# Performance work log

Measured on AMD Instinct MI355X. Metric: run time of the kernel, lower is better.

The kernel has to match this reference:

```python
import jax, jax.numpy as jnp
import numpy as np

EPS = 1e-8

def setup_inputs() -> dict:
    key = jax.random.key(0)
    k1, k2, k3 = jax.random.split(key, 3)
    b, c, h, w = 64, 20, 128, 128
    x = jax.random.normal(k1, (b, c, h, w), dtype=jnp.float32)
    y = jax.random.randint(k2, (b, c), 0, 2).astype(jnp.int32)
    threshold_p = jnp.zeros((b, c, h * w), dtype=jnp.float32)
    fg = jax.random.uniform(k3, (b, c), dtype=jnp.float32)
    return {"x": x, "y": y, "threshold_p": threshold_p, "fg": fg, "iter": 0}

def reference(x, y, threshold_p, fg, iter):
    b, c, h, w = x.shape
    hw = h * w
    xs = jax.nn.sigmoid(x.reshape(b, c, hw))  # [b,c,hw]
    yf = y.astype(xs.dtype)
    if iter % 100 < 80:
        # per-row descending sort, pick the fg*(h*w)-th value as threshold
        srt = -jnp.sort(-xs.reshape(b * c, hw), axis=1)  # descending
        idx = (fg.reshape(-1) * hw).astype(jnp.int32)  # [b*c]
        thr = jnp.take_along_axis(srt, idx[:, None], axis=1).reshape(b, c, 1)
        thr = jax.lax.stop_gradient(thr)
    else:
        thr = jax.nn.sigmoid(jnp.mean(threshold_p.reshape(b, c, hw), axis=2))[:, :, None]
        xs = jax.lax.stop_gradient(xs)
    thr = jnp.clip(thr, 0.0001)  # [b,c,1], broadcasts over hw
    y_ = yf[:, :, None]  # [b,c,1] broadcast equivalent of stacking hw copies
    mask_low = jax.lax.stop_gradient((xs <= thr).astype(xs.dtype) * y_)
    mask_high = jax.lax.stop_gradient((xs > thr).astype(xs.dtype) * y_)
    h_low = (-(xs * xs) / (thr * thr) + 2.0 * xs / thr) * mask_low
    alpha = 1.0 / jnp.clip((1.0 - thr) ** 2, EPS)
    h_high = alpha * (1.0 - xs) * (1.0 - 2.0 * thr + xs) * mask_high
    if iter % 100 < 80:
        neg_loss = -(1.0 - y_) * jnp.log(jnp.clip(1.0 - xs, EPS))
        loss = jnp.mean(h_high + h_low + neg_loss)
    else:
        loss = jnp.sum(h_low) / jnp.sum(mask_low) + jnp.sum(h_high) / jnp.sum(mask_high)
    return loss
```

## Files before the change

kernel.cpp:

```cpp
#include <hip/hip_runtime.h>

#define HW     16384
#define NROWS  1280
#define NT     512
#define NWAVES (NT / 64)
#define CAP    1536
#define MAXB   128

__device__ __forceinline__ unsigned f2u(float f) {
    unsigned u = __float_as_uint(f);
    unsigned m = (unsigned)((int)u >> 31);
    return u ^ (m | 0x80000000u);
}
__device__ __forceinline__ float u2f(unsigned u) {
    u = (u & 0x80000000u) ? (u & 0x7fffffffu) : ~u;
    return __uint_as_float(u);
}

__device__ __forceinline__ float norminv(float p) {
    const float a1=-3.969683028665376e+01f,a2=2.209460984245205e+02f,
                a3=-2.759285104469687e+02f,a4=1.383577518672690e+02f,
                a5=-3.066479806614716e+01f,a6=2.506628277459239e+00f;
    const float b1=-5.447609879822406e+01f,b2=1.615858368580409e+02f,
                b3=-1.556989798598866e+02f,b4=6.680131188771972e+01f,
                b5=-1.328068155288572e+01f;
    const float c1=-7.784894002430293e-03f,c2=-3.223964580411365e-01f,
                c3=-2.400758277161838e+00f,c4=-2.549732539343734e+00f,
                c5=4.374664141464968e+00f,c6=2.938163982698783e+00f;
    const float d1=7.784695709041462e-03f,d2=3.224671290700398e-01f,
                d3=2.445134137142996e+00f,d4=3.754408661907416e+00f;
    const float plow = 0.02425f;
    float q, r;
    if (p < plow) {
        q = sqrtf(-2.f * logf(p));
        return (((((c1*q+c2)*q+c3)*q+c4)*q+c5)*q+c6) /
               ((((d1*q+d2)*q+d3)*q+d4)*q+1.f);
    } else if (p <= 1.f - plow) {
        q = p - 0.5f; r = q * q;
        return (((((a1*r+a2)*r+a3)*r+a4)*r+a5)*r+a6)*q /
               (((((b1*r+b2)*r+b3)*r+b4)*r+b5)*r+1.f);
    } else {
        q = sqrtf(-2.f * logf(1.f - p));
        return -(((((c1*q+c2)*q+c3)*q+c4)*q+c5)*q+c6) /
                ((((d1*q+d2)*q+d3)*q+d4)*q+1.f);
    }
}

__device__ __forceinline__ void block_scan_pick(
    const unsigned* h, int bpl, unsigned kk,
    volatile unsigned* s_bin, volatile unsigned* s_k, unsigned* wtot)
{
    const int tid  = threadIdx.x;
    const int lane = tid & 63;
    const int wid  = tid >> 6;
    const int base = tid * bpl;
    unsigned local = 0;
    for (int j = 0; j < bpl; ++j) local += h[base + j];
    unsigned s = local;
    #pragma unroll
    for (int off = 1; off < 64; off <<= 1) {
        unsigned t = __shfl_down(s, off, 64);
        if (lane + off < 64) s += t;
    }
    if (lane == 0) wtot[wid] = s;
    __syncthreads();
    unsigned aw = 0;
    #pragma unroll
    for (int w = 0; w < NWAVES; ++w) if (w > wid) aw += wtot[w];
    const unsigned above = aw + (s - local);
    if (above <= kk && above + local > kk) {
        unsigned run = above;
        for (int j = bpl - 1; j >= 0; --j) {
            unsigned c = h[base + j];
            if (run + c > kk) { *s_bin = (unsigned)(base + j); *s_k = kk - run; break; }
            run += c;
        }
    }
    __syncthreads();
}

__global__ __launch_bounds__(NT) void spatial_bce_row(
    const float* __restrict__ x, const int* __restrict__ y,
    const float* __restrict__ fg, double* __restrict__ partial)
{
    __shared__ unsigned hist[4096];
    __shared__ unsigned buf[CAP];
    __shared__ unsigned buf2[MAXB];
    __shared__ unsigned wtot[NWAVES];
    __shared__ unsigned s_cnt, s_cnt2, s_bin, s_k, s_val;
    __shared__ float    swf[NWAVES][6];
    __shared__ double   swd[NWAVES];

    const int row  = blockIdx.x;
    const int tid  = threadIdx.x;
    const int lane = tid & 63;
    const int wid  = tid >> 6;
    const float4* x4 = (const float4*)(x + (size_t)row * HW);
    const float L2E   = 1.44269504f;
    const float LN2   = 0.69314718f;
    const float NLCAP = 18.420680744f;

    const int yrow = y[row];

    if (yrow == 0) {
        float a0 = 0.f, a1 = 0.f, a2 = 0.f, a3 = 0.f;
        for (int i = tid; i < HW / 4; i += NT) {
            float4 v = x4[i];
            a0 += fminf(fmaxf(v.x, 0.f) + LN2 * log2f(1.f + exp2f(-L2E * fabsf(v.x))), NLCAP);
            a1 += fminf(fmaxf(v.y, 0.f) + LN2 * log2f(1.f + exp2f(-L2E * fabsf(v.y))), NLCAP);
            a2 += fminf(fmaxf(v.z, 0.f) + LN2 * log2f(1.f + exp2f(-L2E * fabsf(v.z))), NLCAP);
            a3 += fminf(fmaxf(v.w, 0.f) + LN2 * log2f(1.f + exp2f(-L2E * fabsf(v.w))), NLCAP);
        }
        double acc = (double)((a0 + a1) + (a2 + a3));
        #pragma unroll
        for (int off = 32; off > 0; off >>= 1) acc += __shfl_down(acc, off, 64);
        if (lane == 0) swd[wid] = acc;
        __syncthreads();
        if (tid == 0) {
            double t = 0.0;
            for (int w = 0; w < NWAVES; ++w) t += swd[w];
            partial[row] = t;
        }
        return;
    }

    int k = (int)(fg[row] * (float)HW);
    k = max(0, min(HW - 1, k));
    const unsigned ku = (unsigned)k;
    const float pq  = 1.f - ((float)k + 0.5f) * (1.f / (float)HW);
    const float z   = norminv(pq);
    const float phi = 0.39894228f * exp2f(-0.72134752f * z * z);
    const float sig = sqrtf(pq * (1.f - pq) * (1.f / (float)HW)) / phi;
    const float dl  = 6.f * sig + 0.02f;
    const float fa  = z + dl, fb = z - dl;
    const unsigned ua = f2u(fa), ub = f2u(fb);

    {
        uint4 zz = {0u, 0u, 0u, 0u};
        for (int i = tid; i < 1024 / 4; i += NT) ((uint4*)hist)[i] = zz;
    }
    if (tid == 0) { s_cnt = 0u; s_cnt2 = 0u; }
    __syncthreads();

    float t1a = 0.f, t2a = 0.f, gaa = 0.f, g2aa = 0.f, cafa = 0.f, cbfa = 0.f;
    float t1b = 0.f, t2b = 0.f, gab = 0.f, g2ab = 0.f, cafb = 0.f, cbfb = 0.f;
    for (int i = tid; i < HW / 4; i += 2 * NT) {
        float4 v0 = x4[i];
        float4 v1 = x4[i + NT];
        float e0[4] = {v0.x, v0.y, v0.z, v0.w};
        float e1[4] = {v1.x, v1.y, v1.z, v1.w};
        #pragma unroll
        for (int j = 0; j < 4; ++j) {
            float xv = e0[j];
            unsigned u = f2u(xv);
            float s = __builtin_amdgcn_rcpf(1.f + exp2f(-L2E * xv));
            float s2 = s * s;
            t1a += s; t2a += s2;
            if (u > ua) { gaa += s; g2aa += s2; cafa += 1.f; }
            if (u > ub) {
                cbfa += 1.f;
                if (u <= ua) { unsigned p = atomicAdd(&s_cnt, 1u); if (p < CAP) buf[p] = u; }
            }
        }
        #pragma unroll
        for (int j = 0; j < 4; ++j) {
            float xv = e1[j];
            unsigned u = f2u(xv);
            float s = __builtin_amdgcn_rcpf(1.f + exp2f(-L2E * xv));
            float s2 = s * s;
            t1b += s; t2b += s2;
            if (u > ua) { gab += s; g2ab += s2; cafb += 1.f; }
            if (u > ub) {
                cbfb += 1.f;
                if (u <= ua) { unsigned p = atomicAdd(&s_cnt, 1u); if (p < CAP) buf[p] = u; }
            }
        }
    }
    float t1 = t1a + t1b, t2 = t2a + t2b;
    float ga = gaa + gab, g2a = g2aa + g2ab;
    float caf = cafa + cafb, cbf = cbfa + cbfb;
    #pragma unroll
    for (int off = 32; off > 0; off >>= 1) {
        t1  += __shfl_down(t1,  off, 64);
        t2  += __shfl_down(t2,  off, 64);
        ga  += __shfl_down(ga,  off, 64);
        g2a += __shfl_down(g2a, off, 64);
        caf += __shfl_down(caf, off, 64);
        cbf += __shfl_down(cbf, off, 64);
    }
    if (lane == 0) {
        swf[wid][0] = t1;  swf[wid][1] = t2;  swf[wid][2] = ga;
        swf[wid][3] = g2a; swf[wid][4] = caf; swf[wid][5] = cbf;
    }
    __syncthreads();
    double dS1 = 0, dS2 = 0, dGa = 0, dG2a = 0, dCa = 0, dCb = 0;
    #pragma unroll
    for (int w = 0; w < NWAVES; ++w) {
        dS1 += swf[w][0]; dS2 += swf[w][1]; dGa  += swf[w][2];
        dG2a += swf[w][3]; dCa += swf[w][4]; dCb += swf[w][5];
    }
    const unsigned ca  = (unsigned)(dCa + 0.5);
    const unsigned cb  = (unsigned)(dCb + 0.5);
    const unsigned cnt = s_cnt;
    const unsigned UCLIP = f2u(-9.2102404f);
    const bool valid = (ca <= ku) && (ku < cb) && (cnt <= CAP);

    unsigned ustar;
    bool addSide;
    float hs = 0.f, hs2 = 0.f, hn = 0.f;

    if (valid) {
        const float scale = 1024.f / (fa - fb);
        for (int c = tid; c < (int)cnt; c += NT) {
            float xv = u2f(buf[c]);
            int bn = (int)((xv - fb) * scale);
            bn = max(0, min(1023, bn));
            atomicAdd(&hist[bn], 1u);
        }
        __syncthreads();
        const unsigned kp = ku - ca;
        block_scan_pick(hist, 1024 / NT, kp, &s_bin, &s_k, wtot);
        const unsigned binv = s_bin;
        const unsigned kin  = s_k;
        for (int c = tid; c < (int)cnt; c += NT) {
            unsigned u = buf[c];
            float xv = u2f(u);
            int bn = (int)((xv - fb) * scale);
            bn = max(0, min(1023, bn));
            if (bn == (int)binv) { unsigned p = atomicAdd(&s_cnt2, 1u); if (p < MAXB) buf2[p] = u; }
        }
        __syncthreads();
        const unsigned m = s_cnt2;
        if (m <= MAXB) {
            for (int i = tid; i < (int)m; i += NT) {
                unsigned v = buf2[i];
                unsigned gt = 0, eq = 0;
                for (int j = 0; j < (int)m; ++j) {
                    unsigned w = buf2[j];
                    gt += (w > v); eq += (w == v);
                }
                if (gt <= kin && kin < gt + eq) s_val = v;
            }
        } else {
            for (int c = tid; c < (int)cnt; c += NT) {
                unsigned v = buf[c];
                unsigned gt = 0, eq = 0;
                for (int j = 0; j < (int)cnt; ++j) {
                    unsigned w = buf[j];
                    gt += (w > v); eq += (w == v);
                }
                if (gt <= kp && kp < gt + eq) s_val = v;
            }
        }
        __syncthreads();
        ustar = s_val;

        if (ustar >= UCLIP) {
            addSide = true;
            for (int c = tid; c < (int)cnt; c += NT) {
                unsigned u = buf[c];
                if (u > ustar) {
                    float xv = u2f(u);
                    float s = __builtin_amdgcn_rcpf(1.f + exp2f(-L2E * xv));
                    hs += s; hs2 += s * s; hn += 1.f;
                }
            }
        } else {
            addSide = false;
            for (int i = tid; i < HW / 4; i += NT) {
                float4 v = x4[i];
                float e[4] = {v.x, v.y, v.z, v.w};
                #pragma unroll
                for (int j = 0; j < 4; ++j) {
                    if (f2u(e[j]) > UCLIP) {
                        float s = __builtin_amdgcn_rcpf(1.f + exp2f(-L2E * e[j]));
                        hs += s; hs2 += s * s; hn += 1.f;
                    }
                }
            }
        }
    } else {
        {
            uint4 zz = {0u, 0u, 0u, 0u};
            for (int i = tid; i < 4096 / 4; i += NT) ((uint4*)hist)[i] = zz;
        }
        __syncthreads();
        for (int i = tid; i < HW / 4; i += NT) {
            float4 v = x4[i];
            atomicAdd(&hist[f2u(v.x) >> 20], 1u);
            atomicAdd(&hist[f2u(v.y) >> 20], 1u);
            atomicAdd(&hist[f2u(v.z) >> 20], 1u);
            atomicAdd(&hist[f2u(v.w) >> 20], 1u);
        }
        __syncthreads();
        block_scan_pick(hist, 4096 / NT, ku, &s_bin, &s_k, wtot);
        const unsigned bin1 = s_bin;
        const unsigned k1   = s_k;
        for (int i = tid; i < 2048; i += NT) hist[i] = 0u;
        __syncthreads();
        for (int i = tid; i < HW / 4; i += NT) {
            float4 v = x4[i];
            unsigned u[4] = {f2u(v.x), f2u(v.y), f2u(v.z), f2u(v.w)};
            #pragma unroll
            for (int j = 0; j < 4; ++j)
                if ((u[j] >> 20) == bin1) atomicAdd(&hist[(u[j] >> 10) & 1023u], 1u);
        }
        __syncthreads();
        block_scan_pick(hist, 1024 / NT, k1, &s_bin, &s_k, wtot);
        const unsigned pfx22 = (bin1 << 10) | s_bin;
        const unsigned k2    = s_k;
        for (int i = tid; i < HW / 4; i += NT) {
            float4 v = x4[i];
            unsigned u[4] = {f2u(v.x), f2u(v.y), f2u(v.z), f2u(v.w)};
            #pragma unroll
            for (int j = 0; j < 4; ++j)
                if ((u[j] >> 10) == pfx22) atomicAdd(&hist[1024 + (u[j] & 1023u)], 1u);
        }
        __syncthreads();
        block_scan_pick(hist + 1024, 1024 / NT, k2, &s_bin, &s_k, wtot);
        ustar = (pfx22 << 10) | s_bin;

        addSide = false;
        const unsigned uthr = max(ustar, UCLIP);
        for (int i = tid; i < HW / 4; i += NT) {
            float4 v = x4[i];
            float e[4] = {v.x, v.y, v.z, v.w};
            #pragma unroll
            for (int j = 0; j < 4; ++j) {
                if (f2u(e[j]) > uthr) {
                    float s = __builtin_amdgcn_rcpf(1.f + exp2f(-L2E * e[j]));
                    hs += s; hs2 += s * s; hn += 1.f;
                }
            }
        }
    }

    #pragma unroll
    for (int off = 32; off > 0; off >>= 1) {
        hs  += __shfl_down(hs,  off, 64);
        hs2 += __shfl_down(hs2, off, 64);
        hn  += __shfl_down(hn,  off, 64);
    }
    if (lane == 0) { swf[wid][0] = hs; swf[wid][1] = hs2; swf[wid][2] = hn; }
    __syncthreads();
    if (tid == 0) {
        double HS = 0, HS2 = 0, HN = 0;
        for (int w = 0; w < NWAVES; ++w) {
            HS += swf[w][0]; HS2 += swf[w][1]; HN += swf[w][2];
        }
        double SH, S2H, NH;
        if (addSide) { SH = dGa + HS; S2H = dG2a + HS2; NH = dCa + HN; }
        else         { SH = HS;       S2H = HS2;        NH = HN; }
        const double SL = dS1 - SH, S2L = dS2 - S2H;

        const float xk = u2f(ustar);
        float thrf = 1.0f / (1.0f + expf(-xk));
        thrf = fmaxf(thrf, 1e-4f);
        const double t   = (double)thrf;
        const double omt = 1.0 - t;
        const double al  = 1.0 / fmax(omt * omt, 1e-8);
        partial[row] = 2.0 * SL / t - S2L / (t * t)
                     + al * (NH * (1.0 - 2.0 * t) + 2.0 * t * SH - S2H);
    }
}

__global__ __launch_bounds__(256) void spatial_bce_final(
    const double* __restrict__ partial, float* __restrict__ out)
{
    __shared__ double sred[256];
    double acc = 0.0;
    for (int i = threadIdx.x; i < NROWS; i += 256) acc += partial[i];
    sred[threadIdx.x] = acc;
    __syncthreads();
    for (int off = 128; off > 0; off >>= 1) {
        if (threadIdx.x < off) sred[threadIdx.x] += sred[threadIdx.x + off];
        __syncthreads();
    }
    if (threadIdx.x == 0)
        out[0] = (float)(sred[0] / ((double)NROWS * (double)HW));
}

extern "C" void kernel_launch(void* const* d_in, const int* in_sizes, int n_in,
                              void* d_out, int out_size, void* d_ws, size_t ws_size,
                              hipStream_t stream) {
    const float* x  = (const float*)d_in[0];
    const int*   y  = (const int*)d_in[1];
    const float* fg = (const float*)d_in[3];

    double* partial = (double*)d_ws;

    spatial_bce_row<<<NROWS, NT, 0, stream>>>(x, y, fg, partial);
    spatial_bce_final<<<1, 256, 0, stream>>>(partial, (float*)d_out);
}
```

Baseline: 38.38 us.

## Split each row across two blocks with a candidate-buffer finalize kernel

Replaces the single per-row kernel with a two-stage scheme. A streaming pass runs two 256-thread blocks per row, each computing partial sigmoid moments and collecting bracket candidates into global memory. A finalize kernel then selects the k-th value from the merged candidates. A monolithic fallback kernel with a replicated radix histogram is kept for when the workspace is too small. The goal is more blocks in flight for better occupancy and bandwidth, at the cost of an extra kernel launch and global round-trips for moments and candidates.

```diff
diff --git a/kernel.cpp b/kernel.cpp
--- a/kernel.cpp
+++ b/kernel.cpp
@@ -2,10 +2,8 @@
 
 #define HW     16384
 #define NROWS  1280
-#define NT     512
-#define NWAVES (NT / 64)
-#define CAP    1536
-#define MAXB   128
+#define CAPH   1024
+#define MB     256
 
 __device__ __forceinline__ unsigned f2u(float f) {
     unsigned u = __float_as_uint(f);
@@ -46,16 +44,30 @@
     }
 }
 
+__device__ __forceinline__ void bracket_ab(int k, float* fa, float* fb) {
+    const float pq  = 1.f - ((float)k + 0.5f) * (1.f / (float)HW);
+    const float z   = norminv(pq);
+    const float phi = 0.39894228f * exp2f(-0.72134752f * z * z);
+    const float sig = sqrtf(pq * (1.f - pq) * (1.f / (float)HW)) / phi;
+    const float dl  = 6.f * sig + 0.02f;
+    *fa = z + dl; *fb = z - dl;
+}
+
+template<int NTH>
 __device__ __forceinline__ void block_scan_pick(
-    const unsigned* h, int bpl, unsigned kk,
+    const unsigned* h, int bpl, int stride, unsigned kk,
     volatile unsigned* s_bin, volatile unsigned* s_k, unsigned* wtot)
 {
+    constexpr int NW = NTH / 64;
     const int tid  = threadIdx.x;
     const int lane = tid & 63;
     const int wid  = tid >> 6;
     const int base = tid * bpl;
     unsigned local = 0;
-    for (int j = 0; j < bpl; ++j) local += h[base + j];
+    for (int j = 0; j < bpl; ++j) {
+        int b = base + j;
+        local += h[stride * b] + (stride == 2 ? h[stride * b + 1] : 0u);
+    }
     unsigned s = local;
     #pragma unroll
     for (int off = 1; off < 64; off <<= 1) {
@@ -66,45 +78,44 @@
     __syncthreads();
     unsigned aw = 0;
     #pragma unroll
-    for (int w = 0; w < NWAVES; ++w) if (w > wid) aw += wtot[w];
+    for (int w = 0; w < NW; ++w) if (w > wid) aw += wtot[w];
     const unsigned above = aw + (s - local);
     if (above <= kk && above + local > kk) {
         unsigned run = above;
         for (int j = bpl - 1; j >= 0; --j) {
-            unsigned c = h[base + j];
-            if (run + c > kk) { *s_bin = (unsigned)(base + j); *s_k = kk - run; break; }
+            int b = base + j;
+            unsigned c = h[stride * b] + (stride == 2 ? h[stride * b + 1] : 0u);
+            if (run + c > kk) { *s_bin = (unsigned)b; *s_k = kk - run; break; }
             run += c;
         }
     }
     __syncthreads();
 }
 
-__global__ __launch_bounds__(NT) void spatial_bce_row(
+__global__ __launch_bounds__(256) void stream_pass(
     const float* __restrict__ x, const int* __restrict__ y,
-    const float* __restrict__ fg, double* __restrict__ partial)
+    const float* __restrict__ fg, double* __restrict__ mom,
+    unsigned* __restrict__ cnts, unsigned* __restrict__ cand)
 {
-    __shared__ unsigned hist[4096];
-    __shared__ unsigned buf[CAP];
-    __shared__ unsigned buf2[MAXB];
-    __shared__ unsigned wtot[NWAVES];
-    __shared__ unsigned s_cnt, s_cnt2, s_bin, s_k, s_val;
-    __shared__ float    swf[NWAVES][6];
-    __shared__ double   swd[NWAVES];
-
-    const int row  = blockIdx.x;
+    __shared__ unsigned sbuf[CAPH];
+    __shared__ unsigned s_cnt;
+    __shared__ float    swf[4][6];
+    __shared__ double   swd[4];
+
+    const int bid  = blockIdx.x;
+    const int row  = bid >> 1;
+    const int half = bid & 1;
     const int tid  = threadIdx.x;
     const int lane = tid & 63;
     const int wid  = tid >> 6;
-    const float4* x4 = (const float4*)(x + (size_t)row * HW);
+    const float4* x4 = (const float4*)(x + (size_t)row * HW + half * (HW / 2));
     const float L2E   = 1.44269504f;
     const float LN2   = 0.69314718f;
     const float NLCAP = 18.420680744f;
 
-    const int yrow = y[row];
-
-    if (yrow == 0) {
+    if (y[row] == 0) {
         float a0 = 0.f, a1 = 0.f, a2 = 0.f, a3 = 0.f;
-        for (int i = tid; i < HW / 4; i += NT) {
+        for (int i = tid; i < HW / 8; i += 256) {
             float4 v = x4[i];
             a0 += fminf(fmaxf(v.x, 0.f) + LN2 * log2f(1.f + exp2f(-L2E * fabsf(v.x))), NLCAP);
             a1 += fminf(fmaxf(v.y, 0.f) + LN2 * log2f(1.f + exp2f(-L2E * fabsf(v.y))), NLCAP);
@@ -117,65 +128,53 @@
         if (lane == 0) swd[wid] = acc;
         __syncthreads();
         if (tid == 0) {
-            double t = 0.0;
-            for (int w = 0; w < NWAVES; ++w) t += swd[w];
-            partial[row] = t;
+            double t = swd[0] + swd[1] + swd[2] + swd[3];
+            mom[(size_t)bid * 6] = t;
         }
         return;
     }
 
     int k = (int)(fg[row] * (float)HW);
     k = max(0, min(HW - 1, k));
-    const unsigned ku = (unsigned)k;
-    const float pq  = 1.f - ((float)k + 0.5f) * (1.f / (float)HW);
-    const float z   = norminv(pq);
-    const float phi = 0.39894228f * exp2f(-0.72134752f * z * z);
-    const float sig = sqrtf(pq * (1.f - pq) * (1.f / (float)HW)) / phi;
-    const float dl  = 6.f * sig + 0.02f;
-    const float fa  = z + dl, fb = z - dl;
+    float fa, fb; bracket_ab(k, &fa, &fb);
     const unsigned ua = f2u(fa), ub = f2u(fb);
-
-    {
-        uint4 zz = {0u, 0u, 0u, 0u};
-        for (int i = tid; i < 1024 / 4; i += NT) ((uint4*)hist)[i] = zz;
-    }
-    if (tid == 0) { s_cnt = 0u; s_cnt2 = 0u; }
+    if (tid == 0) s_cnt = 0u;
     __syncthreads();
 
     float t1a = 0.f, t2a = 0.f, gaa = 0.f, g2aa = 0.f, cafa = 0.f, cbfa = 0.f;
     float t1b = 0.f, t2b = 0.f, gab = 0.f, g2ab = 0.f, cafb = 0.f, cbfb = 0.f;
-    for (int i = tid; i < HW / 4; i += 2 * NT) {
+
+#define PROC(xv, T1, T2, GA, G2A, CAF, CBF)                                   \
+    {                                                                         \
+        float _xv = (xv);                                                     \
+        unsigned _u = f2u(_xv);                                               \
+        float _s = __builtin_amdgcn_rcpf(1.f + exp2f(-L2E * _xv));            \
+        float _s2 = _s * _s;                                                  \
+        T1 += _s; T2 += _s2;                                                  \
+        if (_u > ua) { GA += _s; G2A += _s2; CAF += 1.f; }                    \
+        if (_u > ub) {                                                        \
+            CBF += 1.f;                                                       \
+            if (_u <= ua) {                                                   \
+                unsigned _p = atomicAdd(&s_cnt, 1u);                          \
+                if (_p < CAPH) sbuf[_p] = _u;                                 \
+            }                                                                 \
+        }                                                                     \
+    }
+
+    for (int i = tid; i < HW / 8; i += 512) {
         float4 v0 = x4[i];
-        float4 v1 = x4[i + NT];
-        float e0[4] = {v0.x, v0.y, v0.z, v0.w};
-        float e1[4] = {v1.x, v1.y, v1.z, v1.w};
-        #pragma unroll
-        for (int j = 0; j < 4; ++j) {
-            float xv = e0[j];
-            unsigned u = f2u(xv);
-            float s = __builtin_amdgcn_rcpf(1.f + exp2f(-L2E * xv));
-            float s2 = s * s;
-            t1a += s; t2a += s2;
-            if (u > ua) { gaa += s; g2aa += s2; cafa += 1.f; }
-            if (u > ub) {
-                cbfa += 1.f;
-                if (u <= ua) { unsigned p = atomicAdd(&s_cnt, 1u); if (p < CAP) buf[p] = u; }
-            }
-        }
-        #pragma unroll
-        for (int j = 0; j < 4; ++j) {
-            float xv = e1[j];
-            unsigned u = f2u(xv);
-            float s = __builtin_amdgcn_rcpf(1.f + exp2f(-L2E * xv));
-            float s2 = s * s;
-            t1b += s; t2b += s2;
-            if (u > ua) { gab += s; g2ab += s2; cafb += 1.f; }
-            if (u > ub) {
-                cbfb += 1.f;
-                if (u <= ua) { unsigned p = atomicAdd(&s_cnt, 1u); if (p < CAP) buf[p] = u; }
-            }
-        }
-    }
+        float4 v1 = x4[i + 256];
+        PROC(v0.x, t1a, t2a, gaa, g2aa, cafa, cbfa);
+        PROC(v0.y, t1a, t2a, gaa, g2aa, cafa, cbfa);
+        PROC(v0.z, t1a, t2a, gaa, g2aa, cafa, cbfa);
+        PROC(v0.w, t1a, t2a, gaa, g2aa, cafa, cbfa);
+        PROC(v1.x, t1b, t2b, gab, g2ab, cafb, cbfb);
+        PROC(v1.y, t1b, t2b, gab, g2ab, cafb, cbfb);
+        PROC(v1.z, t1b, t2b, gab, g2ab, cafb, cbfb);
+        PROC(v1.w, t1b, t2b, gab, g2ab, cafb, cbfb);
+    }
+#undef PROC
+
     float t1 = t1a + t1b, t2 = t2a + t2b;
     float ga = gaa + gab, g2a = g2aa + g2ab;
     float caf = cafa + cafb, cbf = cbfa + cbfb;
@@ -193,60 +192,110 @@
         swf[wid][3] = g2a; swf[wid][4] = caf; swf[wid][5] = cbf;
     }
     __syncthreads();
-    double dS1 = 0, dS2 = 0, dGa = 0, dG2a = 0, dCa = 0, dCb = 0;
-    #pragma unroll
-    for (int w = 0; w < NWAVES; ++w) {
-        dS1 += swf[w][0]; dS2 += swf[w][1]; dGa  += swf[w][2];
-        dG2a += swf[w][3]; dCa += swf[w][4]; dCb += swf[w][5];
-    }
+    const unsigned cfin = s_cnt;
+    if (tid == 0) {
+        double m0 = 0, m1 = 0, m2 = 0, m3 = 0, m4 = 0, m5 = 0;
+        #pragma unroll
+        for (int w = 0; w < 4; ++w) {
+            m0 += swf[w][0]; m1 += swf[w][1]; m2 += swf[w][2];
+            m3 += swf[w][3]; m4 += swf[w][4]; m5 += swf[w][5];
+        }
+        double* o = mom + (size_t)bid * 6;
+        o[0] = m0; o[1] = m1; o[2] = m2; o[3] = m3; o[4] = m4; o[5] = m5;
+        cnts[bid] = cfin;
+    }
+    const unsigned c = cfin < CAPH ? cfin : CAPH;
+    unsigned* dst = cand + (size_t)bid * CAPH;
+    for (unsigned j = tid; j < c; j += 256) dst[j] = sbuf[j];
+}
+
+__global__ __launch_bounds__(256) void finalize_row(
+    const float* __restrict__ x, const int* __restrict__ y,
+    const float* __restrict__ fg, const double* __restrict__ mom,
+    const unsigned* __restrict__ cnts, const unsigned* __restrict__ cand,
+    double* __restrict__ partial)
+{
+    __shared__ unsigned hist[4096];
+    __shared__ unsigned buf2[MB];
+    __shared__ unsigned wtot[4];
+    __shared__ unsigned s_cnt2, s_bin, s_k, s_val;
+    __shared__ float    swf[4][3];
+
+    const int r    = blockIdx.x;
+    const int tid  = threadIdx.x;
+    const int lane = tid & 63;
+    const int wid  = tid >> 6;
+
+    if (y[r] == 0) {
+        if (tid == 0)
+            partial[r] = mom[(size_t)(2 * r) * 6] + mom[(size_t)(2 * r + 1) * 6];
+        return;
+    }
+
+    const double* mA = mom + (size_t)(2 * r) * 6;
+    const double* mB = mA + 6;
+    const double dS1 = mA[0] + mB[0], dS2 = mA[1] + mB[1];
+    const double dGa = mA[2] + mB[2], dG2a = mA[3] + mB[3];
+    const double dCa = mA[4] + mB[4], dCb = mA[5] + mB[5];
     const unsigned ca  = (unsigned)(dCa + 0.5);
-    const unsigned cb  = (unsigned)(dCb + 0.5);
-    const unsigned cnt = s_cnt;
+    const unsigned cbn = (unsigned)(dCb + 0.5);
+    int k = (int)(fg[r] * (float)HW);
+    k = max(0, min(HW - 1, k));
+    const unsigned ku = (unsigned)k;
+    const unsigned c0 = cnts[2 * r], c1 = cnts[2 * r + 1];
     const unsigned UCLIP = f2u(-9.2102404f);
-    const bool valid = (ca <= ku) && (ku < cb) && (cnt <= CAP);
-
-    unsigned ustar;
-    bool addSide;
-    float hs = 0.f, hs2 = 0.f, hn = 0.f;
+    const bool valid = (ca <= ku) && (ku < cbn) && (c0 <= CAPH) && (c1 <= CAPH);
+    const unsigned* seg0 = cand + (size_t)(2 * r) * CAPH;
+    const unsigned* seg1 = cand + (size_t)(2 * r + 1) * CAPH;
+    const unsigned total = c0 + c1;
+    const float L2E = 1.44269504f;
+
+    unsigned ustar = 0;
+    bool haveU = false;
 
     if (valid) {
+        float fa, fb; bracket_ab(k, &fa, &fb);
         const float scale = 1024.f / (fa - fb);
-        for (int c = tid; c < (int)cnt; c += NT) {
-            float xv = u2f(buf[c]);
-            int bn = (int)((xv - fb) * scale);
+        for (int i = tid; i < 1024; i += 256) hist[i] = 0u;
+        if (tid == 0) s_cnt2 = 0u;
+        __syncthreads();
+        for (unsigned t = tid; t < total; t += 256) {
+            unsigned u = (t < c0) ? seg0[t] : seg1[t - c0];
+            int bn = (int)((u2f(u) - fb) * scale);
             bn = max(0, min(1023, bn));
             atomicAdd(&hist[bn], 1u);
         }
         __syncthreads();
-        const unsigned kp = ku - ca;
-        block_scan_pick(hist, 1024 / NT, kp, &s_bin, &s_k, wtot);
-        const unsigned binv = s_bin;
-        const unsigned kin  = s_k;
-        for (int c = tid; c < (int)cnt; c += NT) {
-            unsigned u = buf[c];
-            float xv = u2f(u);
-            int bn = (int)((xv - fb) * scale);
+        block_scan_pick<256>(hist, 4, 1, ku - ca, &s_bin, &s_k, wtot);
+        const unsigned binv = s_bin, kin = s_k;
+        for (unsigned t = tid; t < total; t += 256) {
+            unsigned u = (t < c0) ? seg0[t] : seg1[t - c0];
+            int bn = (int)((u2f(u) - fb) * scale);
             bn = max(0, min(1023, bn));
-            if (bn == (int)binv) { unsigned p = atomicAdd(&s_cnt2, 1u); if (p < MAXB) buf2[p] = u; }
+            if (bn == (int)binv) {
+                unsigned p = atomicAdd(&s_cnt2, 1u);
+                if (p < MB) buf2[p] = u;
+            }
         }
         __syncthreads();
         const unsigned m = s_cnt2;
-        if (m <= MAXB) {
-            for (int i = tid; i < (int)m; i += NT) {
+        if (m <= MB) {
+            for (unsigned i = tid; i < m; i += 256) {
                 unsigned v = buf2[i];
                 unsigned gt = 0, eq = 0;
-                for (int j = 0; j < (int)m; ++j) {
+                for (unsigned j = 0; j < m; ++j) {
                     unsigned w = buf2[j];
                     gt += (w > v); eq += (w == v);
                 }
                 if (gt <= kin && kin < gt + eq) s_val = v;
             }
         } else {
-            for (int c = tid; c < (int)cnt; c += NT) {
-                unsigned v = buf[c];
+            const unsigned kp = ku - ca;
+            for (unsigned t = tid; t < total; t += 256) {
+                unsigned v = (t < c0) ? seg0[t] : seg1[t - c0];
                 unsigned gt = 0, eq = 0;
-                for (int j = 0; j < (int)cnt; ++j) {
-                    unsigned w = buf[j];
+                for (unsigned j = 0; j < total; ++j) {
+                    unsigned w = (j < c0) ? seg0[j] : seg1[j - c0];
                     gt += (w > v); eq += (w == v);
                 }
                 if (gt <= kp && kp < gt + eq) s_val = v;
@@ -254,75 +303,62 @@
         }
         __syncthreads();
         ustar = s_val;
-
-        if (ustar >= UCLIP) {
-            addSide = true;
-            for (int c = tid; c < (int)cnt; c += NT) {
-                unsigned u = buf[c];
-                if (u > ustar) {
-                    float xv = u2f(u);
-                    float s = __builtin_amdgcn_rcpf(1.f + exp2f(-L2E * xv));
-                    hs += s; hs2 += s * s; hn += 1.f;
-                }
-            }
-        } else {
-            addSide = false;
-            for (int i = tid; i < HW / 4; i += NT) {
+        haveU = true;
+    }
+
+    float hs = 0.f, hs2 = 0.f, hn = 0.f;
+    bool addSide = false;
+    if (haveU && ustar >= UCLIP) {
+        addSide = true;
+        for (unsigned t = tid; t < total; t += 256) {
+            unsigned u = (t < c0) ? seg0[t] : seg1[t - c0];
+            if (u > ustar) {
+                float xv = u2f(u);
+                float s = __builtin_amdgcn_rcpf(1.f + exp2f(-L2E * xv));
+                hs += s; hs2 += s * s; hn += 1.f;
+            }
+        }
+    } else {
+        const float4* x4 = (const float4*)(x + (size_t)r * HW);
+        if (!haveU) {
+            for (int i = tid; i < 4096; i += 256) hist[i] = 0u;
+            __syncthreads();
+            for (int i = tid; i < HW / 4; i += 256) {
                 float4 v = x4[i];
-                float e[4] = {v.x, v.y, v.z, v.w};
+                atomicAdd(&hist[f2u(v.x) >> 20], 1u);
+                atomicAdd(&hist[f2u(v.y) >> 20], 1u);
+                atomicAdd(&hist[f2u(v.z) >> 20], 1u);
+                atomicAdd(&hist[f2u(v.w) >> 20], 1u);
+            }
+            __syncthreads();
+            block_scan_pick<256>(hist, 16, 1, ku, &s_bin, &s_k, wtot);
+            const unsigned bin1 = s_bin, k1 = s_k;
+            for (int i = tid; i < 2048; i += 256) hist[i] = 0u;
+            __syncthreads();
+            for (int i = tid; i < HW / 4; i += 256) {
+                float4 v = x4[i];
+                unsigned uu[4] = {f2u(v.x), f2u(v.y), f2u(v.z), f2u(v.w)};
                 #pragma unroll
-                for (int j = 0; j < 4; ++j) {
-                    if (f2u(e[j]) > UCLIP) {
-                        float s = __builtin_amdgcn_rcpf(1.f + exp2f(-L2E * e[j]));
-                        hs += s; hs2 += s * s; hn += 1.f;
-                    }
-                }
-            }
-        }
-    } else {
-        {
-            uint4 zz = {0u, 0u, 0u, 0u};
-            for (int i = tid; i < 4096 / 4; i += NT) ((uint4*)hist)[i] = zz;
-        }
-        __syncthreads();
-        for (int i = tid; i < HW / 4; i += NT) {
-            float4 v = x4[i];
-            atomicAdd(&hist[f2u(v.x) >> 20], 1u);
-            atomicAdd(&hist[f2u(v.y) >> 20], 1u);
-            atomicAdd(&hist[f2u(v.z) >> 20], 1u);
-            atomicAdd(&hist[f2u(v.w) >> 20], 1u);
-        }
-        __syncthreads();
-        block_scan_pick(hist, 4096 / NT, ku, &s_bin, &s_k, wtot);
-        const unsigned bin1 = s_bin;
-        const unsigned k1   = s_k;
-        for (int i = tid; i < 2048; i += NT) hist[i] = 0u;
-        __syncthreads();
-        for (int i = tid; i < HW / 4; i += NT) {
-            float4 v = x4[i];
-            unsigned u[4] = {f2u(v.x), f2u(v.y), f2u(v.z), f2u(v.w)};
-            #pragma unroll
-            for (int j = 0; j < 4; ++j)
-                if ((u[j] >> 20) == bin1) atomicAdd(&hist[(u[j] >> 10) & 1023u], 1u);
-        }
-        __syncthreads();
-        block_scan_pick(hist, 1024 / NT, k1, &s_bin, &s_k, wtot);
-        const unsigned pfx22 = (bin1 << 10) | s_bin;
-        const unsigned k2    = s_k;
-        for (int i = tid; i < HW / 4; i += NT) {
-            float4 v = x4[i];
-            unsigned u[4] = {f2u(v.x), f2u(v.y), f2u(v.z), f2u(v.w)};
-            #pragma unroll
-            for (int j = 0; j < 4; ++j)
-                if ((u[j] >> 10) == pfx22) atomicAdd(&hist[1024 + (u[j] & 1023u)], 1u);
-        }
-        __syncthreads();
-        block_scan_pick(hist + 1024, 1024 / NT, k2, &s_bin, &s_k, wtot);
-        ustar = (pfx22 << 10) | s_bin;
-
-        addSide = false;
-        const unsigned uthr = max(ustar, UCLIP);
-        for (int i = tid; i < HW / 4; i += NT) {
+                for (int j = 0; j < 4; ++j)
+                    if ((uu[j] >> 20) == bin1) atomicAdd(&hist[(uu[j] >> 10) & 1023u], 1u);
+            }
+            __syncthreads();
+            block_scan_pick<256>(hist, 4, 1, k1, &s_bin, &s_k, wtot);
+            const unsigned pfx22 = (bin1 << 10) | s_bin;
+            const unsigned k2 = s_k;
+            for (int i = tid; i < HW / 4; i += 256) {
+                float4 v = x4[i];
+                unsigned uu[4] = {f2u(v.x), f2u(v.y), f2u(v.z), f2u(v.w)};
+                #pragma unroll
+                for (int j = 0; j < 4; ++j)
+                    if ((uu[j] >> 10) == pfx22) atomicAdd(&hist[1024 + (uu[j] & 1023u)], 1u);
+            }
+            __syncthreads();
+            block_scan_pick<256>(hist + 1024, 4, 1, k2, &s_bin, &s_k, wtot);
+            ustar = (pfx22 << 10) | s_bin;
+        }
+        const unsigned uthr = ustar > UCLIP ? ustar : UCLIP;
+        for (int i = tid; i < HW / 4; i += 256) {
             float4 v = x4[i];
             float e[4] = {v.x, v.y, v.z, v.w};
             #pragma unroll
@@ -345,26 +381,26 @@
     __syncthreads();
     if (tid == 0) {
         double HS = 0, HS2 = 0, HN = 0;
-        for (int w = 0; w < NWAVES; ++w) {
+        #pragma unroll
+        for (int w = 0; w < 4; ++w) {
             HS += swf[w][0]; HS2 += swf[w][1]; HN += swf[w][2];
         }
         double SH, S2H, NH;
         if (addSide) { SH = dGa + HS; S2H = dG2a + HS2; NH = dCa + HN; }
         else         { SH = HS;       S2H = HS2;        NH = HN; }
         const double SL = dS1 - SH, S2L = dS2 - S2H;
-
         const float xk = u2f(ustar);
         float thrf = 1.0f / (1.0f + expf(-xk));
         thrf = fmaxf(thrf, 1e-4f);
         const double t   = (double)thrf;
         const double omt = 1.0 - t;
         const double al  = 1.0 / fmax(omt * omt, 1e-8);
-        partial[row] = 2.0 * SL / t - S2L / (t * t)
-                     + al * (NH * (1.0 - 2.0 * t) + 2.0 * t * SH - S2H);
-    }
-}
-
-__global__ __launch_bounds__(256) void spatial_bce_final(
+        partial[r] = 2.0 * SL / t - S2L / (t * t)
+                   + al * (NH * (1.0 - 2.0 * t) + 2.0 * t * SH - S2H);
+    }
+}
+
+__global__ __launch_bounds__(256) void final_reduce(
     const double* __restrict__ partial, float* __restrict__ out)
 {
     __shared__ double sred[256];
@@ -380,6 +416,199 @@
         out[0] = (float)(sred[0] / ((double)NROWS * (double)HW));
 }
 
+__global__ __launch_bounds__(512) void mono_row(
+    const float* __restrict__ x, const int* __restrict__ y,
+    const float* __restrict__ fg, double* __restrict__ partial)
+{
+    __shared__ unsigned hist[4096 * 2];
+    __shared__ unsigned buf[1024];
+    __shared__ unsigned wtot[8];
+    __shared__ unsigned s_cnt, s_bin, s_k;
+    __shared__ float    swf[8][5];
+    __shared__ double   swd[8];
+
+    const int row  = blockIdx.x;
+    const int tid  = threadIdx.x;
+    const int lane = tid & 63;
+    const int wid  = tid >> 6;
+    const float4* x4 = (const float4*)(x + (size_t)row * HW);
+    const float L2E   = 1.44269504f;
+    const float LN2   = 0.69314718f;
+    const float NLCAP = 18.420680744f;
+
+    const int yrow = y[row];
+
+    if (yrow == 0) {
+        float a0 = 0.f, a1 = 0.f, a2 = 0.f, a3 = 0.f;
+        for (int i = tid; i < HW / 4; i += 512) {
+            float4 v = x4[i];
+            a0 += fminf(fmaxf(v.x, 0.f) + LN2 * log2f(1.f + exp2f(-L2E * fabsf(v.x))), NLCAP);
+            a1 += fminf(fmaxf(v.y, 0.f) + LN2 * log2f(1.f + exp2f(-L2E * fabsf(v.y))), NLCAP);
+            a2 += fminf(fmaxf(v.z, 0.f) + LN2 * log2f(1.f + exp2f(-L2E * fabsf(v.z))), NLCAP);
+            a3 += fminf(fmaxf(v.w, 0.f) + LN2 * log2f(1.f + exp2f(-L2E * fabsf(v.w))), NLCAP);
+        }
+        double acc = (double)((a0 + a1) + (a2 + a3));
+        #pragma unroll
+        for (int off = 32; off > 0; off >>= 1) acc += __shfl_down(acc, off, 64);
+        if (lane == 0) swd[wid] = acc;
+        __syncthreads();
+        if (tid == 0) {
+            double t = 0.0;
+            for (int w = 0; w < 8; ++w) t += swd[w];
+            partial[row] = t;
+        }
+        return;
+    }
+
+    {
+        uint4 z = {0u, 0u, 0u, 0u};
+        for (int i = tid; i < 4096 * 2 / 4; i += 512) ((uint4*)hist)[i] = z;
+    }
+    if (tid == 0) {
+        int k = (int)(fg[row] * (float)HW);
+        k = max(0, min(HW - 1, k));
+        s_k = (unsigned)k; s_cnt = 0u;
+    }
+    __syncthreads();
+    const unsigned k0 = s_k;
+
+    const int rep = tid & 1;
+    for (int i = tid; i < HW / 4; i += 1024) {
+        float4 v0 = x4[i];
+        float4 v1 = x4[i + 512];
+        atomicAdd(&hist[2 * (f2u(v0.x) >> 20) + rep], 1u);
+        atomicAdd(&hist[2 * (f2u(v0.y) >> 20) + rep], 1u);
+        atomicAdd(&hist[2 * (f2u(v0.z) >> 20) + rep], 1u);
+        atomicAdd(&hist[2 * (f2u(v0.w) >> 20) + rep], 1u);
+        atomicAdd(&hist[2 * (f2u(v1.x) >> 20) + rep], 1u);
+        atomicAdd(&hist[2 * (f2u(v1.y) >> 20) + rep], 1u);
+        atomicAdd(&hist[2 * (f2u(v1.z) >> 20) + rep], 1u);
+        atomicAdd(&hist[2 * (f2u(v1.w) >> 20) + rep], 1u);
+    }
+    __syncthreads();
+    block_scan_pick<512>(hist, 4096 / 512, 2, k0, &s_bin, &s_k, wtot);
+    const unsigned bin1 = s_bin;
+    const unsigned k1   = s_k;
+
+    for (int i = tid; i < 2048; i += 512) hist[i] = 0u;
+    float sL = 0.f, s2L = 0.f, sH = 0.f, s2H = 0.f;
+    int nH = 0;
+    for (int i = tid; i < HW / 4; i += 512) {
+        float4 v = x4[i];
+        float e[4] = {v.x, v.y, v.z, v.w};
+        #pragma unroll
+        for (int j = 0; j < 4; ++j) {
+            float xv = e[j];
+            unsigned u = f2u(xv);
+            unsigned b = u >> 20;
+            if (b == bin1) {
+                unsigned p = atomicAdd(&s_cnt, 1u);
+                if (p < 1024) buf[p] = u;
+            } else {
+                float s = __builtin_amdgcn_rcpf(1.f + exp2f(-L2E * xv));
+                float s2 = s * s;
+                if (b > bin1) { sH += s; s2H += s2; ++nH; }
+                else          { sL += s; s2L += s2; }
+            }
+        }
+    }
+    __syncthreads();
+    const unsigned cnt = s_cnt;
+
+    unsigned ustar;
+    if (cnt <= 1024) {
+        for (int c = tid; c < (int)cnt; c += 512)
+            atomicAdd(&hist[(buf[c] >> 10) & 1023u], 1u);
+        __syncthreads();
+        block_scan_pick<512>(hist, 2, 1, k1, &s_bin, &s_k, wtot);
+        const unsigned pfx22 = (bin1 << 10) | s_bin;
+        const unsigned k2    = s_k;
+        for (int c = tid; c < (int)cnt; c += 512)
+            if ((buf[c] >> 10) == pfx22) atomicAdd(&hist[1024 + (buf[c] & 1023u)], 1u);
+        __syncthreads();
+        block_scan_pick<512>(hist + 1024, 2, 1, k2, &s_bin, &s_k, wtot);
+        ustar = (pfx22 << 10) | s_bin;
+    } else {
+        for (int i = tid; i < HW / 4; i += 512) {
+            float4 v = x4[i];
+            unsigned uu[4] = {f2u(v.x), f2u(v.y), f2u(v.z), f2u(v.w)};
+            #pragma unroll
+            for (int j = 0; j < 4; ++j)
+                if ((uu[j] >> 20) == bin1) atomicAdd(&hist[(uu[j] >> 10) & 1023u], 1u);
+        }
+        __syncthreads();
+        block_scan_pick<512>(hist, 2, 1, k1, &s_bin, &s_k, wtot);
+        const unsigned pfx22 = (bin1 << 10) | s_bin;
+        const unsigned k2    = s_k;
+        for (int i = tid; i < HW / 4; i += 512) {
+            float4 v = x4[i];
+            unsigned uu[4] = {f2u(v.x), f2u(v.y), f2u(v.z), f2u(v.w)};
+            #pragma unroll
+            for (int j = 0; j < 4; ++j)
+                if ((uu[j] >> 10) == pfx22) atomicAdd(&hist[1024 + (uu[j] & 1023u)], 1u);
+        }
+        __syncthreads();
+        block_scan_pick<512>(hist + 1024, 2, 1, k2, &s_bin, &s_k, wtot);
+        ustar = (pfx22 << 10) | s_bin;
+    }
+
+    const float xk = u2f(ustar);
+    float thr = 1.0f / (1.0f + expf(-xk));
+    thr = fmaxf(thr, 1e-4f);
+
+    if (cnt <= 1024) {
+        for (int c = tid; c < (int)cnt; c += 512) {
+            float xv = u2f(buf[c]);
+            float s  = __builtin_amdgcn_rcpf(1.f + exp2f(-L2E * xv));
+            float s2 = s * s;
+            if (s > thr) { sH += s; s2H += s2; ++nH; }
+            else         { sL += s; s2L += s2; }
+        }
+    } else {
+        for (int i = tid; i < HW / 4; i += 512) {
+            float4 v = x4[i];
+            float e[4] = {v.x, v.y, v.z, v.w};
+            #pragma unroll
+            for (int j = 0; j < 4; ++j) {
+                unsigned u = f2u(e[j]);
+                if ((u >> 20) == bin1) {
+                    float s  = __builtin_amdgcn_rcpf(1.f + exp2f(-L2E * e[j]));
+                    float s2 = s * s;
+                    if (s > thr) { sH += s; s2H += s2; ++nH; }
+                    else         { sL += s; s2L += s2; }
+                }
+            }
+        }
+    }
+
+    float nHf = (float)nH;
+    #pragma unroll
+    for (int off = 32; off > 0; off >>= 1) {
+        sL  += __shfl_down(sL,  off, 64);
+        s2L += __shfl_down(s2L, off, 64);
+        sH  += __shfl_down(sH,  off, 64);
+        s2H += __shfl_down(s2H, off, 64);
+        nHf += __shfl_down(nHf, off, 64);
+    }
+    if (lane == 0) {
+        swf[wid][0] = sL; swf[wid][1] = s2L; swf[wid][2] = sH;
+        swf[wid][3] = s2H; swf[wid][4] = nHf;
+    }
+    __syncthreads();
+    if (tid == 0) {
+        double SL = 0, S2L = 0, SH = 0, S2H = 0, NH = 0;
+        for (int w = 0; w < 8; ++w) {
+            SL += swf[w][0]; S2L += swf[w][1]; SH += swf[w][2];
+            S2H += swf[w][3]; NH += (double)swf[w][4];
+        }
+        const double t   = (double)thr;
+        const double omt = 1.0 - t;
+        const double al  = 1.0 / fmax(omt * omt, 1e-8);
+        partial[row] = 2.0 * SL / t - S2L / (t * t)
+                     + al * (NH * (1.0 - 2.0 * t) + 2.0 * t * SH - S2H);
+    }
+}
+
 extern "C" void kernel_launch(void* const* d_in, const int* in_sizes, int n_in,
                               void* d_out, int out_size, void* d_ws, size_t ws_size,
                               hipStream_t stream) {
@@ -387,8 +616,23 @@
     const int*   y  = (const int*)d_in[1];
     const float* fg = (const float*)d_in[3];
 
-    double* partial = (double*)d_ws;
-
-    spatial_bce_row<<<NROWS, NT, 0, stream>>>(x, y, fg, partial);
-    spatial_bce_final<<<1, 256, 0, stream>>>(partial, (float*)d_out);
-}
+    const size_t offPartial = 0;
+    const size_t offMom     = offPartial + (size_t)NROWS * 8;
+    const size_t offCnts    = offMom + (size_t)2 * NROWS * 6 * 8;
+    const size_t offCand    = offCnts + (size_t)2 * NROWS * 4;
+    const size_t need       = offCand + (size_t)2 * NROWS * CAPH * 4;
+
+    double* partial = (double*)((char*)d_ws + offPartial);
+
+    if (ws_size >= need) {
+        double*   mom  = (double*)((char*)d_ws + offMom);
+        unsigned* cnts = (unsigned*)((char*)d_ws + offCnts);
+        unsigned* cand = (unsigned*)((char*)d_ws + offCand);
+        stream_pass <<<2 * NROWS, 256, 0, stream>>>(x, y, fg, mom, cnts, cand);
+        finalize_row<<<NROWS,     256, 0, stream>>>(x, y, fg, mom, cnts, cand, partial);
+        final_reduce<<<1,         256, 0, stream>>>(partial, (float*)d_out);
+    } else {
+        mono_row    <<<NROWS, 512, 0, stream>>>(x, y, fg, partial);
+        final_reduce<<<1,     256, 0, stream>>>(partial, (float*)d_out);
+    }
+}
```

After: 39.57 us. 1.03x slower.
